# Kernel optimization log

Hardware: AMD Instinct MI355X
Metric: run time of the kernel (lower is better)

The kernel has to match this reference:

```python
import jax, jax.numpy as jnp
import numpy as np

D_STATE = 8
DT_RANK = 8  # ceil(128/16)


def _grouped_1x1(x, w):
    # x: (B,H,W,Cin), w: (g, Cout//g, Cin//g)
    B, H, W, _ = x.shape
    g, o, i = w.shape
    xg = x.reshape(B, H, W, g, i)
    return jnp.einsum('bhwgi,goi->bhwgo', xg, w).reshape(B, H, W, g * o)


def setup_inputs() -> dict:
    key = jax.random.key(0)
    ks = jax.random.split(key, 16)
    B, H, W, C = 8, 64, 64, 128
    g = 4
    D = 128  # expand_dim = d_inner
    N = D_STATE
    R = DT_RANK
    inp = {}
    inp['x'] = jax.random.normal(ks[0], (B, H, W, C), dtype=jnp.float32)
    inp['w1'] = jax.random.normal(ks[1], (g, D // g, C // g), dtype=jnp.float32) * 0.1
    inp['dw'] = jax.random.normal(ks[2], (3, 3, 1, D), dtype=jnp.float32) * 0.1  # HWIO depthwise
    inp['in_proj_w'] = jax.random.normal(ks[3], (2 * D, D), dtype=jnp.float32) * 0.05
    inp['conv1d_w'] = jax.random.normal(ks[4], (D, 3), dtype=jnp.float32) * 0.1
    inp['conv1d_b'] = jax.random.normal(ks[5], (D,), dtype=jnp.float32) * 0.05
    inp['x_proj_w'] = jax.random.normal(ks[6], (R + 2 * N, D), dtype=jnp.float32) * 0.05
    inp['dt_proj_w'] = jax.random.normal(ks[7], (D, R), dtype=jnp.float32) * 0.05
    inp['dt_proj_b'] = jax.random.normal(ks[8], (D,), dtype=jnp.float32) * 0.05
    inp['A_log'] = jnp.log(jnp.tile(jnp.arange(1, N + 1, dtype=jnp.float32)[None, :], (D, 1)))
    inp['D_param'] = jnp.ones((D,), dtype=jnp.float32)
    inp['out_proj_w'] = jax.random.normal(ks[9], (D, D), dtype=jnp.float32) * 0.05
    inp['gamma'] = jnp.ones((D,), dtype=jnp.float32)
    inp['beta'] = jnp.zeros((D,), dtype=jnp.float32)
    inp['w2'] = jax.random.normal(ks[10], (g, D // g, C // g), dtype=jnp.float32) * 0.1
    inp['wout'] = jax.random.normal(ks[11], (g, C // g, D // g), dtype=jnp.float32) * 0.1
    return inp


def _mamba(x_seq, in_proj_w, conv1d_w, conv1d_b, x_proj_w, dt_proj_w, dt_proj_b, A_log, D_param, out_proj_w):
    # x_seq: (B, L, D)
    B, L, D = x_seq.shape
    N, R = D_STATE, DT_RANK
    xz = jnp.einsum('bld,ed->ble', x_seq, in_proj_w)  # (B,L,2D)
    u, z = xz[..., :D], xz[..., D:]
    # causal depthwise conv1d, kernel=3, left pad 2 (torch: padding=2, slice [:L])
    up = jnp.pad(u, ((0, 0), (2, 0), (0, 0)))
    u = (up[:, 0:L] * conv1d_w[:, 0] + up[:, 1:L + 1] * conv1d_w[:, 1]
         + up[:, 2:L + 2] * conv1d_w[:, 2] + conv1d_b)
    u = jax.nn.silu(u)
    x_dbl = jnp.einsum('bld,ed->ble', u, x_proj_w)  # (B,L,R+2N)
    dt = x_dbl[..., :R]
    Bm = x_dbl[..., R:R + N]
    Cm = x_dbl[..., R + N:]
    delta = jax.nn.softplus(jnp.einsum('blr,dr->bld', dt, dt_proj_w) + dt_proj_b)  # (B,L,D)
    A = -jnp.exp(A_log)  # (D,N)

    def step(h, inp):
        d_t, u_t, b_t, c_t = inp  # (B,D),(B,D),(B,N),(B,N)
        dA = jnp.exp(d_t[..., None] * A)            # (B,D,N)
        h = dA * h + (d_t * u_t)[..., None] * b_t[:, None, :]
        y_t = jnp.einsum('bdn,bn->bd', h, c_t)
        return h, y_t

    h0 = jnp.zeros((B, D, N), dtype=x_seq.dtype)
    xs = (jnp.swapaxes(delta, 0, 1), jnp.swapaxes(u, 0, 1),
          jnp.swapaxes(Bm, 0, 1), jnp.swapaxes(Cm, 0, 1))
    _, ys = jax.lax.scan(step, h0, xs)              # ys: (L,B,D)
    y = jnp.swapaxes(ys, 0, 1) + u * D_param
    y = y * jax.nn.silu(z)
    return jnp.einsum('bld,ed->ble', y, out_proj_w)


def reference(x, w1, dw, in_proj_w, conv1d_w, conv1d_b, x_proj_w, dt_proj_w, dt_proj_b,
              A_log, D_param, out_proj_w, gamma, beta, w2, wout):
    B, H, W, C = x.shape
    D = dw.shape[-1]
    x1 = _grouped_1x1(x, w1)  # (B,H,W,D)
    x1 = jax.lax.conv_general_dilated(
        x1, dw, window_strides=(1, 1), padding='SAME',
        feature_group_count=D, dimension_numbers=('NHWC', 'HWIO', 'NHWC'))
    x1 = jax.nn.silu(x1)
    x1_seq = x1.reshape(B, H * W, D)
    x1_seq = _mamba(x1_seq, in_proj_w, conv1d_w, conv1d_b, x_proj_w,
                    dt_proj_w, dt_proj_b, A_log, D_param, out_proj_w)
    x1 = x1_seq.reshape(B, H, W, D)
    mu = jnp.mean(x1, axis=-1, keepdims=True)
    var = jnp.mean(jnp.square(x1 - mu), axis=-1, keepdims=True)
    x1 = (x1 - mu) * jax.lax.rsqrt(var + 1e-5) * gamma + beta
    x2 = jax.nn.silu(_grouped_1x1(x, w2))
    x_fuse = x1 * x2
    return _grouped_1x1(x_fuse, wout)  # (B,H,W,C)
```

## Files before the change

### kernel.cpp

```cpp
#include <hip/hip_runtime.h>
#include <math.h>

#define B_    8
#define C_    128
#define D_    128
#define L_    4096
#define NPOS_ 32768
#define NC_   256
#define S_    16
#define MFL_  1048576

typedef __attribute__((ext_vector_type(8))) short short8;
typedef __attribute__((ext_vector_type(4))) float f32x4;

__device__ __forceinline__ float siluf(float x) { return x / (1.f + __expf(-x)); }
__device__ __forceinline__ float softplusf(float x) {
    if (x > 20.f) return x;
    return __logf(1.f + __expf(x));
}
__device__ __forceinline__ unsigned short f2bf(float f) {
    unsigned int u = __float_as_uint(f);
    u = (u + 0x7FFFu + ((u >> 16) & 1u)) >> 16;
    return (unsigned short)u;
}
__device__ __forceinline__ float bf2f(unsigned short h) {
    return __uint_as_float(((unsigned int)h) << 16);
}
__device__ __forceinline__ void scan_as(float dl, const float* Ar, bool fast, float* a) {
    if (fast) {
        float e1 = __expf(-dl);
        a[0] = e1;
        a[1] = e1 * e1;
        a[2] = a[1] * e1;
        a[3] = a[1] * a[1];
        a[4] = a[3] * e1;
        a[5] = a[3] * a[1];
        a[6] = a[5] * e1;
        a[7] = a[3] * a[3];
    } else {
        #pragma unroll
        for (int n = 0; n < 8; ++n) a[n] = __expf(dl * Ar[n]);
    }
}

__global__ __launch_bounds__(256) void k0_cvt(const float* __restrict__ inW,
                                              const float* __restrict__ OW,
                                              const float* __restrict__ xpw,
                                              unsigned short* __restrict__ inWb,
                                              unsigned short* __restrict__ OWb,
                                              unsigned short* __restrict__ xpwb) {
    for (int i = blockIdx.x * 256 + threadIdx.x; i < 52224; i += gridDim.x * 256) {
        if (i < 32768)      inWb[i] = f2bf(inW[i]);
        else if (i < 49152) OWb[i - 32768] = f2bf(OW[i - 32768]);
        else                xpwb[i - 49152] = f2bf(xpw[i - 49152]);
    }
}

__global__ __launch_bounds__(256) void k1_g1x1(const float* __restrict__ x,
                                               const float* __restrict__ w1,
                                               const float* __restrict__ w2,
                                               unsigned short* __restrict__ t1b,
                                               unsigned short* __restrict__ x2sb) {
    __shared__ float xs[16 * 128];
    int t = threadIdx.x;
    int d = t & 127, ph = t >> 7;
    int g = d >> 5, o = d & 31;
    float w1r[32], w2r[32];
    #pragma unroll
    for (int i = 0; i < 32; ++i) {
        w1r[i] = w1[g * 1024 + o * 32 + i];
        w2r[i] = w2[g * 1024 + o * 32 + i];
    }
    int pos0 = blockIdx.x * 32;
    for (int it = 0; it < 2; ++it) {
        int p0 = pos0 + it * 16;
        #pragma unroll
        for (int q = 0; q < 2; ++q) {
            int fi = t * 2 + q;
            *(float4*)&xs[fi * 4] = *(const float4*)&x[p0 * 128 + fi * 4];
        }
        __syncthreads();
        #pragma unroll
        for (int q = 0; q < 8; ++q) {
            int pl = ph * 8 + q;
            float a1 = 0.f, a2 = 0.f;
            const float* xr = &xs[pl * 128 + g * 32];
            #pragma unroll
            for (int i4 = 0; i4 < 8; ++i4) {
                float4 xv = *(const float4*)&xr[i4 * 4];
                a1 += xv.x * w1r[i4*4] + xv.y * w1r[i4*4+1] + xv.z * w1r[i4*4+2] + xv.w * w1r[i4*4+3];
                a2 += xv.x * w2r[i4*4] + xv.y * w2r[i4*4+1] + xv.z * w2r[i4*4+2] + xv.w * w2r[i4*4+3];
            }
            int pos = p0 + pl;
            t1b[pos * 128 + d]  = f2bf(a1);
            x2sb[pos * 128 + d] = f2bf(siluf(a2));
        }
        __syncthreads();
    }
}

__global__ __launch_bounds__(128) void k2_dwconv(const unsigned short* __restrict__ t1b,
                                                 const float* __restrict__ dw,
                                                 unsigned short* __restrict__ x1cb) {
    int d = threadIdx.x;
    float dwr[9];
    #pragma unroll
    for (int k = 0; k < 9; ++k) dwr[k] = dw[k * 128 + d];
    int bid = blockIdx.x;
    int wt = bid & 15, ht = (bid >> 4) & 7, b = bid >> 7;
    int h0 = ht * 8, w0 = wt * 4;
    float rows[10][6];
    #pragma unroll
    for (int r = 0; r < 10; ++r) {
        int hh = h0 - 1 + r;
        bool hv = (hh >= 0) && (hh < 64);
        #pragma unroll
        for (int c = 0; c < 6; ++c) {
            int w = w0 - 1 + c;
            bool wvv = (w >= 0) && (w < 64);
            rows[r][c] = (hv && wvv) ? bf2f(t1b[((b * 64 + hh) * 64 + w) * 128 + d]) : 0.f;
        }
    }
    #pragma unroll
    for (int hi = 0; hi < 8; ++hi) {
        #pragma unroll
        for (int wi = 0; wi < 4; ++wi) {
            float acc = rows[hi][wi]     * dwr[0] + rows[hi][wi+1]   * dwr[1] + rows[hi][wi+2]   * dwr[2]
                      + rows[hi+1][wi]   * dwr[3] + rows[hi+1][wi+1] * dwr[4] + rows[hi+1][wi+2] * dwr[5]
                      + rows[hi+2][wi]   * dwr[6] + rows[hi+2][wi+1] * dwr[7] + rows[hi+2][wi+2] * dwr[8];
            x1cb[((b * 64 + h0 + hi) * 64 + w0 + wi) * 128 + d] = f2bf(siluf(acc));
        }
    }
}

__global__ __launch_bounds__(256) void k3_mfma(const unsigned short* __restrict__ Abf,
                                               const unsigned short* __restrict__ Bbf,
                                               unsigned short* __restrict__ urawb,
                                               unsigned short* __restrict__ zb) {
    __shared__ unsigned short Al[64 * 72];
    __shared__ unsigned short Bl[128 * 72];
    int t = threadIdx.x;
    int pos0 = (blockIdx.x >> 1) * 64;
    int half = blockIdx.x & 1;
    const unsigned short* Bh = Bbf + (size_t)half * 128 * 128;
    unsigned short* dst = half ? zb : urawb;
    int lane = t & 63, wv = t >> 6;
    int lanem = lane & 15, laneq = lane >> 4;
    f32x4 acc[8];
    #pragma unroll
    for (int i = 0; i < 8; ++i) acc[i] = (f32x4){0.f, 0.f, 0.f, 0.f};
    for (int kc = 0; kc < 2; ++kc) {
        #pragma unroll
        for (int q = 0; q < 2; ++q) {
            int c = t + q * 256;
            int row = c >> 3, col = c & 7;
            *(int4*)&Al[row * 72 + col * 8] = *(const int4*)&Abf[(pos0 + row) * 128 + kc * 64 + col * 8];
        }
        #pragma unroll
        for (int q = 0; q < 4; ++q) {
            int c = t + q * 256;
            int row = c >> 3, col = c & 7;
            *(int4*)&Bl[row * 72 + col * 8] = *(const int4*)&Bh[row * 128 + kc * 64 + col * 8];
        }
        __syncthreads();
        #pragma unroll
        for (int ks = 0; ks < 2; ++ks) {
            short8 af = *(const short8*)&Al[(wv * 16 + lanem) * 72 + ks * 32 + laneq * 8];
            #pragma unroll
            for (int ni = 0; ni < 8; ++ni) {
                short8 bfr = *(const short8*)&Bl[(ni * 16 + lanem) * 72 + ks * 32 + laneq * 8];
                acc[ni] = __builtin_amdgcn_mfma_f32_16x16x32_bf16(af, bfr, acc[ni], 0, 0, 0);
            }
        }
        __syncthreads();
    }
    #pragma unroll
    for (int ni = 0; ni < 8; ++ni)
        #pragma unroll
        for (int r = 0; r < 4; ++r) {
            int m = pos0 + wv * 16 + laneq * 4 + r;
            int n = ni * 16 + lanem;
            dst[m * 128 + n] = f2bf(acc[ni][r]);
        }
}

__global__ __launch_bounds__(256) void k4_convproj(const unsigned short* __restrict__ urawb,
                                                   const float* __restrict__ cw,
                                                   const float* __restrict__ cb,
                                                   const unsigned short* __restrict__ xpwb,
                                                   const float* __restrict__ dtw,
                                                   const float* __restrict__ dtb,
                                                   unsigned short* __restrict__ usb,
                                                   float* __restrict__ delta,
                                                   float* __restrict__ Bm,
                                                   float* __restrict__ Cm) {
    __shared__ unsigned short uA[32 * 136];
    __shared__ unsigned short xB[32 * 136];
    __shared__ float xdb[32 * 36];
    int t = threadIdx.x;
    int d = t & 127, ph = t >> 7;
    for (int i = t; i < 32 * 128; i += 256) {
        int n = i >> 7, k = i & 127;
        xB[n * 136 + k] = (n < 24) ? xpwb[n * 128 + k] : (unsigned short)0;
    }
    float cw0 = cw[d * 3 + 0], cw1 = cw[d * 3 + 1], cw2 = cw[d * 3 + 2], cbr = cb[d];
    float dtwr[8];
    #pragma unroll
    for (int r = 0; r < 8; ++r) dtwr[r] = dtw[d * 8 + r];
    float dtbr = dtb[d];

    int gpos0 = blockIdx.x * 32;
    int ll0 = (gpos0 & 4095) + ph * 16;
    int base = (gpos0 + ph * 16) * 128 + d;
    float ur0 = (ll0 >= 2) ? bf2f(urawb[base - 256]) : 0.f;
    float ur1 = (ll0 >= 1) ? bf2f(urawb[base - 128]) : 0.f;
    #pragma unroll
    for (int q = 0; q < 16; ++q) {
        float urq = bf2f(urawb[base + q * 128]);
        float v = siluf(ur0 * cw0 + ur1 * cw1 + urq * cw2 + cbr);
        unsigned short vb = f2bf(v);
        usb[base + q * 128] = vb;
        uA[(ph * 16 + q) * 136 + d] = vb;
        ur0 = ur1; ur1 = urq;
    }
    __syncthreads();
    int lane = t & 63, wv = t >> 6;
    int lanem = lane & 15, laneq = lane >> 4;
    int m0 = (wv & 1) * 16, n0 = (wv >> 1) * 16;
    f32x4 accx = (f32x4){0.f, 0.f, 0.f, 0.f};
    #pragma unroll
    for (int ks = 0; ks < 4; ++ks) {
        short8 af  = *(const short8*)&uA[(m0 + lanem) * 136 + ks * 32 + laneq * 8];
        short8 bfr = *(const short8*)&xB[(n0 + lanem) * 136 + ks * 32 + laneq * 8];
        accx = __builtin_amdgcn_mfma_f32_16x16x32_bf16(af, bfr, accx, 0, 0, 0);
    }
    #pragma unroll
    for (int r = 0; r < 4; ++r)
        xdb[(m0 + laneq * 4 + r) * 36 + n0 + lanem] = accx[r];
    __syncthreads();
    #pragma unroll
    for (int q = 0; q < 16; ++q) {
        int pl = ph * 16 + q;
        float dt = dtbr;
        #pragma unroll
        for (int r = 0; r < 8; ++r) dt += xdb[pl * 36 + r] * dtwr[r];
        delta[base + q * 128] = softplusf(dt);
    }
    for (int i = t; i < 512; i += 256) {
        int p = i >> 4, j = i & 15;
        float v = xdb[p * 36 + 8 + j];
        int gp = gpos0 + p;
        if (j < 8) Bm[gp * 8 + j] = v;
        else       Cm[gp * 8 + (j - 8)] = v;
    }
}

__global__ __launch_bounds__(128) void k5_scan1(const float* __restrict__ delta,
                                                const unsigned short* __restrict__ usb,
                                                const float* __restrict__ Bm,
                                                const float* __restrict__ A_log,
                                                float* __restrict__ cA,
                                                float* __restrict__ cB) {
    int d = threadIdx.x;
    int bc = blockIdx.x;
    int b = bc >> 8, c = bc & 255;
    float Ar[8]; bool fast = true;
    #pragma unroll
    for (int n = 0; n < 8; ++n) {
        Ar[n] = -__expf(A_log[d * 8 + n]);
        fast = fast && (fabsf(Ar[n] + (float)(n + 1)) < 2e-3f);
    }
    float h[8], ap[8];
    #pragma unroll
    for (int n = 0; n < 8; ++n) { h[n] = 0.f; ap[n] = 1.f; }
    int base  = (b * L_ + c * S_) * 128 + d;
    int bbase = (b * L_ + c * S_) * 8;
    #pragma unroll
    for (int s = 0; s < S_; ++s) {
        float dl = delta[base + s * 128];
        float uv = bf2f(usb[base + s * 128]);
        float du = dl * uv;
        float4 bm0 = *(const float4*)&Bm[bbase + s * 8];
        float4 bm1 = *(const float4*)&Bm[bbase + s * 8 + 4];
        float a[8];
        scan_as(dl, Ar, fast, a);
        ap[0] *= a[0]; h[0] = a[0] * h[0] + du * bm0.x;
        ap[1] *= a[1]; h[1] = a[1] * h[1] + du * bm0.y;
        ap[2] *= a[2]; h[2] = a[2] * h[2] + du * bm0.z;
        ap[3] *= a[3]; h[3] = a[3] * h[3] + du * bm0.w;
        ap[4] *= a[4]; h[4] = a[4] * h[4] + du * bm1.x;
        ap[5] *= a[5]; h[5] = a[5] * h[5] + du * bm1.y;
        ap[6] *= a[6]; h[6] = a[6] * h[6] + du * bm1.z;
        ap[7] *= a[7]; h[7] = a[7] * h[7] + du * bm1.w;
    }
    int obase = ((b * NC_ + c) * 128 + d) * 8;
    *(float4*)&cA[obase]     = make_float4(ap[0], ap[1], ap[2], ap[3]);
    *(float4*)&cA[obase + 4] = make_float4(ap[4], ap[5], ap[6], ap[7]);
    *(float4*)&cB[obase]     = make_float4(h[0], h[1], h[2], h[3]);
    *(float4*)&cB[obase + 4] = make_float4(h[4], h[5], h[6], h[7]);
}

__global__ __launch_bounds__(128) void k6_scan2(const float* __restrict__ cA,
                                                const float* __restrict__ cB,
                                                float* __restrict__ carry) {
    int b = blockIdx.x >> 3;
    int slice = blockIdx.x & 7;
    int dn = slice * 128 + threadIdx.x;
    float h = 0.f;
    #pragma unroll 4
    for (int c = 0; c < NC_; ++c) {
        int idx = (b * NC_ + c) * 1024 + dn;
        float a  = cA[idx];
        float bv = cB[idx];
        carry[idx] = h;
        h = a * h + bv;
    }
}

__global__ __launch_bounds__(128) void k7_scan3(const float* __restrict__ delta,
                                                const unsigned short* __restrict__ usb,
                                                const float* __restrict__ Bm,
                                                const float* __restrict__ Cm,
                                                const unsigned short* __restrict__ zb,
                                                const float* __restrict__ A_log,
                                                const float* __restrict__ Dp,
                                                const float* __restrict__ carry,
                                                unsigned short* __restrict__ ybf) {
    int d = threadIdx.x;
    int bc = blockIdx.x;
    int b = bc >> 8, c = bc & 255;
    float Ar[8]; bool fast = true;
    #pragma unroll
    for (int n = 0; n < 8; ++n) {
        Ar[n] = -__expf(A_log[d * 8 + n]);
        fast = fast && (fabsf(Ar[n] + (float)(n + 1)) < 2e-3f);
    }
    float Dpr = Dp[d];
    int cbase = ((b * NC_ + c) * 128 + d) * 8;
    float4 h0 = *(const float4*)&carry[cbase];
    float4 h1 = *(const float4*)&carry[cbase + 4];
    float h[8] = {h0.x, h0.y, h0.z, h0.w, h1.x, h1.y, h1.z, h1.w};
    int base  = (b * L_ + c * S_) * 128 + d;
    int bbase = (b * L_ + c * S_) * 8;
    #pragma unroll
    for (int s = 0; s < S_; ++s) {
        float dl = delta[base + s * 128];
        float uv = bf2f(usb[base + s * 128]);
        float zv = bf2f(zb[base + s * 128]);
        float du = dl * uv;
        float4 bm0 = *(const float4*)&Bm[bbase + s * 8];
        float4 bm1 = *(const float4*)&Bm[bbase + s * 8 + 4];
        float4 cm0 = *(const float4*)&Cm[bbase + s * 8];
        float4 cm1 = *(const float4*)&Cm[bbase + s * 8 + 4];
        float a[8];
        scan_as(dl, Ar, fast, a);
        h[0] = a[0] * h[0] + du * bm0.x;
        h[1] = a[1] * h[1] + du * bm0.y;
        h[2] = a[2] * h[2] + du * bm0.z;
        h[3] = a[3] * h[3] + du * bm0.w;
        h[4] = a[4] * h[4] + du * bm1.x;
        h[5] = a[5] * h[5] + du * bm1.y;
        h[6] = a[6] * h[6] + du * bm1.z;
        h[7] = a[7] * h[7] + du * bm1.w;
        float yv = h[0] * cm0.x + h[1] * cm0.y + h[2] * cm0.z + h[3] * cm0.w
                 + h[4] * cm1.x + h[5] * cm1.y + h[6] * cm1.z + h[7] * cm1.w;
        yv = (yv + uv * Dpr) * siluf(zv);
        ybf[base + s * 128] = f2bf(yv);
    }
}

__global__ __launch_bounds__(256) void k8a_mfma(const unsigned short* __restrict__ Abf,
                                                const unsigned short* __restrict__ Bbf,
                                                unsigned short* __restrict__ xzb) {
    __shared__ unsigned short Al[64 * 72];
    __shared__ unsigned short Bl[128 * 72];
    int t = threadIdx.x;
    int pos0 = blockIdx.x * 64;
    int lane = t & 63, wv = t >> 6;
    int lanem = lane & 15, laneq = lane >> 4;
    f32x4 acc[8];
    #pragma unroll
    for (int i = 0; i < 8; ++i) acc[i] = (f32x4){0.f, 0.f, 0.f, 0.f};
    for (int kc = 0; kc < 2; ++kc) {
        #pragma unroll
        for (int q = 0; q < 2; ++q) {
            int c = t + q * 256;
            int row = c >> 3, col = c & 7;
            *(int4*)&Al[row * 72 + col * 8] = *(const int4*)&Abf[(pos0 + row) * 128 + kc * 64 + col * 8];
        }
        #pragma unroll
        for (int q = 0; q < 4; ++q) {
            int c = t + q * 256;
            int row = c >> 3, col = c & 7;
            *(int4*)&Bl[row * 72 + col * 8] = *(const int4*)&Bbf[row * 128 + kc * 64 + col * 8];
        }
        __syncthreads();
        #pragma unroll
        for (int ks = 0; ks < 2; ++ks) {
            short8 af = *(const short8*)&Al[(wv * 16 + lanem) * 72 + ks * 32 + laneq * 8];
            #pragma unroll
            for (int ni = 0; ni < 8; ++ni) {
                short8 bfr = *(const short8*)&Bl[(ni * 16 + lanem) * 72 + ks * 32 + laneq * 8];
                acc[ni] = __builtin_amdgcn_mfma_f32_16x16x32_bf16(af, bfr, acc[ni], 0, 0, 0);
            }
        }
        __syncthreads();
    }
    #pragma unroll
    for (int ni = 0; ni < 8; ++ni)
        #pragma unroll
        for (int r = 0; r < 4; ++r) {
            int m = pos0 + wv * 16 + laneq * 4 + r;
            int n = ni * 16 + lanem;
            xzb[m * 128 + n] = f2bf(acc[ni][r]);
        }
}

__global__ __launch_bounds__(256) void k8b_epi(const unsigned short* __restrict__ xzb,
                                               const float* __restrict__ gamma,
                                               const float* __restrict__ beta,
                                               const unsigned short* __restrict__ x2sb,
                                               const float* __restrict__ wout,
                                               float* __restrict__ out) {
    __shared__ float woutL[4 * 1160];
    __shared__ float gbL[256];
    int t = threadIdx.x;
    int pos0 = blockIdx.x * 64;
    for (int idx = t; idx < 4096; idx += 256) {
        int g = idx >> 10, r = idx & 1023, o = r >> 5, i = r & 31;
        woutL[g * 1160 + o * 36 + i] = wout[idx];
    }
    if (t < 128) gbL[t] = gamma[t];
    else         gbL[t] = beta[t - 128];
    __syncthreads();

    int g = t & 3, pos = t >> 2;
    int gpos = pos0 + pos;
    float v[32];
    #pragma unroll
    for (int i4 = 0; i4 < 8; ++i4) {
        ushort4 xv = *(const ushort4*)&xzb[gpos * 128 + g * 32 + i4 * 4];
        v[i4*4+0] = bf2f(xv.x); v[i4*4+1] = bf2f(xv.y);
        v[i4*4+2] = bf2f(xv.z); v[i4*4+3] = bf2f(xv.w);
    }
    float s = 0.f, s2 = 0.f;
    #pragma unroll
    for (int i = 0; i < 32; ++i) { s += v[i]; s2 += v[i] * v[i]; }
    s  += __shfl_xor(s, 1, 64);  s  += __shfl_xor(s, 2, 64);
    s2 += __shfl_xor(s2, 1, 64); s2 += __shfl_xor(s2, 2, 64);
    float m = s * (1.f / 128.f);
    float var = s2 * (1.f / 128.f) - m * m;
    float rstd = rsqrtf(var + 1e-5f);
    #pragma unroll
    for (int i4 = 0; i4 < 8; ++i4) {
        ushort4 xv = *(const ushort4*)&x2sb[gpos * 128 + g * 32 + i4 * 4];
        unsigned short xa[4] = {xv.x, xv.y, xv.z, xv.w};
        #pragma unroll
        for (int k = 0; k < 4; ++k) {
            int e = g * 32 + i4 * 4 + k;
            float vv = (v[i4 * 4 + k] - m) * rstd * gbL[e] + gbL[128 + e];
            v[i4 * 4 + k] = vv * bf2f(xa[k]);
        }
    }
    const float* wg = &woutL[g * 1160];
    int obase = gpos * 128 + g * 32;
    #pragma unroll
    for (int ob = 0; ob < 8; ++ob) {
        float o4[4];
        #pragma unroll
        for (int oo = 0; oo < 4; ++oo) {
            int o = ob * 4 + oo;
            float acc = 0.f;
            #pragma unroll
            for (int i4 = 0; i4 < 8; ++i4) {
                float4 wv4 = *(const float4*)&wg[o * 36 + i4 * 4];
                acc += v[i4*4] * wv4.x + v[i4*4+1] * wv4.y
                     + v[i4*4+2] * wv4.z + v[i4*4+3] * wv4.w;
            }
            o4[oo] = acc;
        }
        *(float4*)&out[obase + ob * 4] = make_float4(o4[0], o4[1], o4[2], o4[3]);
    }
}

extern "C" void kernel_launch(void* const* d_in, const int* in_sizes, int n_in,
                              void* d_out, int out_size, void* d_ws, size_t ws_size,
                              hipStream_t stream) {
    (void)in_sizes; (void)n_in; (void)out_size; (void)ws_size;
    const float* x         = (const float*)d_in[0];
    const float* w1        = (const float*)d_in[1];
    const float* dw        = (const float*)d_in[2];
    const float* in_proj_w = (const float*)d_in[3];
    const float* conv1d_w  = (const float*)d_in[4];
    const float* conv1d_b  = (const float*)d_in[5];
    const float* x_proj_w  = (const float*)d_in[6];
    const float* dt_proj_w = (const float*)d_in[7];
    const float* dt_proj_b = (const float*)d_in[8];
    const float* A_log     = (const float*)d_in[9];
    const float* D_param   = (const float*)d_in[10];
    const float* out_proj_w= (const float*)d_in[11];
    const float* gamma     = (const float*)d_in[12];
    const float* beta      = (const float*)d_in[13];
    const float* w2        = (const float*)d_in[14];
    const float* wout      = (const float*)d_in[15];
    float* out = (float*)d_out;

    float* ws = (float*)d_ws;
    unsigned short* x2sb  = (unsigned short*)(ws);
    unsigned short* t1b   = (unsigned short*)(ws + 2  * (size_t)MFL_);
    unsigned short* x1cb  = (unsigned short*)(ws + 4  * (size_t)MFL_);
    unsigned short* urawb = (unsigned short*)(ws + 6  * (size_t)MFL_);
    unsigned short* zb    = (unsigned short*)(ws + 8  * (size_t)MFL_);
    unsigned short* ybf   = (unsigned short*)(ws + 10 * (size_t)MFL_);
    unsigned short* xzb   = (unsigned short*)(ws + 12 * (size_t)MFL_);
    unsigned short* usb   = (unsigned short*)(ws + 14 * (size_t)MFL_);
    float* delta = ws + 16 * (size_t)MFL_;
    float* Bm    = ws + 20 * (size_t)MFL_;
    float* Cm    = Bm + (size_t)NPOS_ * 8;
    float* cA    = Cm + (size_t)NPOS_ * 8;
    float* cB    = cA + 2 * (size_t)MFL_;
    float* carry = cB + 2 * (size_t)MFL_;
    unsigned short* inWb = (unsigned short*)(carry + 2 * (size_t)MFL_);
    unsigned short* OWb  = inWb + 32768;
    unsigned short* xpwb = OWb + 16384;

    k0_cvt<<<64, 256, 0, stream>>>(in_proj_w, out_proj_w, x_proj_w, inWb, OWb, xpwb);
    k1_g1x1<<<1024, 256, 0, stream>>>(x, w1, w2, t1b, x2sb);
    k2_dwconv<<<1024, 128, 0, stream>>>(t1b, dw, x1cb);
    k3_mfma<<<1024, 256, 0, stream>>>(x1cb, inWb, urawb, zb);
    k4_convproj<<<1024, 256, 0, stream>>>(urawb, conv1d_w, conv1d_b, xpwb,
                                          dt_proj_w, dt_proj_b, usb, delta, Bm, Cm);
    k5_scan1<<<2048, 128, 0, stream>>>(delta, usb, Bm, A_log, cA, cB);
    k6_scan2<<<64, 128, 0, stream>>>(cA, cB, carry);
    k7_scan3<<<2048, 128, 0, stream>>>(delta, usb, Bm, Cm, zb, A_log, D_param, carry, ybf);
    k8a_mfma<<<512, 256, 0, stream>>>(ybf, OWb, xzb);
    k8b_epi<<<512, 256, 0, stream>>>(xzb, gamma, beta, x2sb, wout, out);
}
```

Measured before the change: 239.6 us.

## Fuse chunk scan pass into conv/projection kernel and fold weight conversion into k1

The first-pass chunk scan (per-chunk decay products and partial states) now runs inside the conv/x_proj kernel. It reuses delta, u and B values already held in registers and shared memory instead of re-reading them from global memory in a separate kernel. The bf16 weight conversion kernel is also folded into the first grouped 1x1 kernel, with a few threads per block doing the conversion. Together these remove two kernel launches and a round of global memory traffic. The costs are more register pressure in the fused kernel and some per-block imbalance in k1.

```diff
diff --git a/kernel.cpp b/kernel.cpp
--- a/kernel.cpp
+++ b/kernel.cpp
@@ -43,26 +43,27 @@
     }
 }
 
-__global__ __launch_bounds__(256) void k0_cvt(const float* __restrict__ inW,
-                                              const float* __restrict__ OW,
-                                              const float* __restrict__ xpw,
-                                              unsigned short* __restrict__ inWb,
-                                              unsigned short* __restrict__ OWb,
-                                              unsigned short* __restrict__ xpwb) {
-    for (int i = blockIdx.x * 256 + threadIdx.x; i < 52224; i += gridDim.x * 256) {
-        if (i < 32768)      inWb[i] = f2bf(inW[i]);
-        else if (i < 49152) OWb[i - 32768] = f2bf(OW[i - 32768]);
-        else                xpwb[i - 49152] = f2bf(xpw[i - 49152]);
-    }
-}
-
 __global__ __launch_bounds__(256) void k1_g1x1(const float* __restrict__ x,
                                                const float* __restrict__ w1,
                                                const float* __restrict__ w2,
+                                               const float* __restrict__ inW,
+                                               const float* __restrict__ OW,
+                                               const float* __restrict__ xpw,
+                                               unsigned short* __restrict__ inWb,
+                                               unsigned short* __restrict__ OWb,
+                                               unsigned short* __restrict__ xpwb,
                                                unsigned short* __restrict__ t1b,
                                                unsigned short* __restrict__ x2sb) {
     __shared__ float xs[16 * 128];
     int t = threadIdx.x;
+    {
+        int i = blockIdx.x * 51 + t;
+        if (t < 51 && i < 52224) {
+            if (i < 32768)      inWb[i] = f2bf(inW[i]);
+            else if (i < 49152) OWb[i - 32768] = f2bf(OW[i - 32768]);
+            else                xpwb[i - 49152] = f2bf(xpw[i - 49152]);
+        }
+    }
     int d = t & 127, ph = t >> 7;
     int g = d >> 5, o = d & 31;
     float w1r[32], w2r[32];
@@ -184,16 +185,19 @@
         }
 }
 
-__global__ __launch_bounds__(256) void k4_convproj(const unsigned short* __restrict__ urawb,
-                                                   const float* __restrict__ cw,
-                                                   const float* __restrict__ cb,
-                                                   const unsigned short* __restrict__ xpwb,
-                                                   const float* __restrict__ dtw,
-                                                   const float* __restrict__ dtb,
-                                                   unsigned short* __restrict__ usb,
-                                                   float* __restrict__ delta,
-                                                   float* __restrict__ Bm,
-                                                   float* __restrict__ Cm) {
+__global__ __launch_bounds__(256) void k45_convproj(const unsigned short* __restrict__ urawb,
+                                                    const float* __restrict__ cw,
+                                                    const float* __restrict__ cb,
+                                                    const unsigned short* __restrict__ xpwb,
+                                                    const float* __restrict__ dtw,
+                                                    const float* __restrict__ dtb,
+                                                    const float* __restrict__ A_log,
+                                                    unsigned short* __restrict__ usb,
+                                                    float* __restrict__ delta,
+                                                    float* __restrict__ Bm,
+                                                    float* __restrict__ Cm,
+                                                    float* __restrict__ cA,
+                                                    float* __restrict__ cB) {
     __shared__ unsigned short uA[32 * 136];
     __shared__ unsigned short xB[32 * 136];
     __shared__ float xdb[32 * 36];
@@ -208,6 +212,12 @@
     #pragma unroll
     for (int r = 0; r < 8; ++r) dtwr[r] = dtw[d * 8 + r];
     float dtbr = dtb[d];
+    float Ar[8]; bool fast = true;
+    #pragma unroll
+    for (int n = 0; n < 8; ++n) {
+        Ar[n] = -__expf(A_log[d * 8 + n]);
+        fast = fast && (fabsf(Ar[n] + (float)(n + 1)) < 2e-3f);
+    }
 
     int gpos0 = blockIdx.x * 32;
     int ll0 = (gpos0 & 4095) + ph * 16;
@@ -238,14 +248,33 @@
     for (int r = 0; r < 4; ++r)
         xdb[(m0 + laneq * 4 + r) * 36 + n0 + lanem] = accx[r];
     __syncthreads();
+    float h[8], ap[8];
+    #pragma unroll
+    for (int n = 0; n < 8; ++n) { h[n] = 0.f; ap[n] = 1.f; }
     #pragma unroll
     for (int q = 0; q < 16; ++q) {
         int pl = ph * 16 + q;
         float dt = dtbr;
         #pragma unroll
         for (int r = 0; r < 8; ++r) dt += xdb[pl * 36 + r] * dtwr[r];
-        delta[base + q * 128] = softplusf(dt);
-    }
+        float dl = softplusf(dt);
+        delta[base + q * 128] = dl;
+        float du = dl * bf2f(uA[pl * 136 + d]);
+        float a[8];
+        scan_as(dl, Ar, fast, a);
+        #pragma unroll
+        for (int n = 0; n < 8; ++n) {
+            ap[n] *= a[n];
+            h[n] = a[n] * h[n] + du * xdb[pl * 36 + 8 + n];
+        }
+    }
+    int bH = gpos0 >> 12;
+    int c  = ((gpos0 & 4095) >> 4) + ph;
+    int obase = ((bH * NC_ + c) * 128 + d) * 8;
+    *(float4*)&cA[obase]     = make_float4(ap[0], ap[1], ap[2], ap[3]);
+    *(float4*)&cA[obase + 4] = make_float4(ap[4], ap[5], ap[6], ap[7]);
+    *(float4*)&cB[obase]     = make_float4(h[0], h[1], h[2], h[3]);
+    *(float4*)&cB[obase + 4] = make_float4(h[4], h[5], h[6], h[7]);
     for (int i = t; i < 512; i += 256) {
         int p = i >> 4, j = i & 15;
         float v = xdb[p * 36 + 8 + j];
@@ -253,51 +282,6 @@
         if (j < 8) Bm[gp * 8 + j] = v;
         else       Cm[gp * 8 + (j - 8)] = v;
     }
-}
-
-__global__ __launch_bounds__(128) void k5_scan1(const float* __restrict__ delta,
-                                                const unsigned short* __restrict__ usb,
-                                                const float* __restrict__ Bm,
-                                                const float* __restrict__ A_log,
-                                                float* __restrict__ cA,
-                                                float* __restrict__ cB) {
-    int d = threadIdx.x;
-    int bc = blockIdx.x;
-    int b = bc >> 8, c = bc & 255;
-    float Ar[8]; bool fast = true;
-    #pragma unroll
-    for (int n = 0; n < 8; ++n) {
-        Ar[n] = -__expf(A_log[d * 8 + n]);
-        fast = fast && (fabsf(Ar[n] + (float)(n + 1)) < 2e-3f);
-    }
-    float h[8], ap[8];
-    #pragma unroll
-    for (int n = 0; n < 8; ++n) { h[n] = 0.f; ap[n] = 1.f; }
-    int base  = (b * L_ + c * S_) * 128 + d;
-    int bbase = (b * L_ + c * S_) * 8;
-    #pragma unroll
-    for (int s = 0; s < S_; ++s) {
-        float dl = delta[base + s * 128];
-        float uv = bf2f(usb[base + s * 128]);
-        float du = dl * uv;
-        float4 bm0 = *(const float4*)&Bm[bbase + s * 8];
-        float4 bm1 = *(const float4*)&Bm[bbase + s * 8 + 4];
-        float a[8];
-        scan_as(dl, Ar, fast, a);
-        ap[0] *= a[0]; h[0] = a[0] * h[0] + du * bm0.x;
-        ap[1] *= a[1]; h[1] = a[1] * h[1] + du * bm0.y;
-        ap[2] *= a[2]; h[2] = a[2] * h[2] + du * bm0.z;
-        ap[3] *= a[3]; h[3] = a[3] * h[3] + du * bm0.w;
-        ap[4] *= a[4]; h[4] = a[4] * h[4] + du * bm1.x;
-        ap[5] *= a[5]; h[5] = a[5] * h[5] + du * bm1.y;
-        ap[6] *= a[6]; h[6] = a[6] * h[6] + du * bm1.z;
-        ap[7] *= a[7]; h[7] = a[7] * h[7] + du * bm1.w;
-    }
-    int obase = ((b * NC_ + c) * 128 + d) * 8;
-    *(float4*)&cA[obase]     = make_float4(ap[0], ap[1], ap[2], ap[3]);
-    *(float4*)&cA[obase + 4] = make_float4(ap[4], ap[5], ap[6], ap[7]);
-    *(float4*)&cB[obase]     = make_float4(h[0], h[1], h[2], h[3]);
-    *(float4*)&cB[obase + 4] = make_float4(h[4], h[5], h[6], h[7]);
 }
 
 __global__ __launch_bounds__(128) void k6_scan2(const float* __restrict__ cA,
@@ -524,13 +508,13 @@
     unsigned short* OWb  = inWb + 32768;
     unsigned short* xpwb = OWb + 16384;
 
-    k0_cvt<<<64, 256, 0, stream>>>(in_proj_w, out_proj_w, x_proj_w, inWb, OWb, xpwb);
-    k1_g1x1<<<1024, 256, 0, stream>>>(x, w1, w2, t1b, x2sb);
+    k1_g1x1<<<1024, 256, 0, stream>>>(x, w1, w2, in_proj_w, out_proj_w, x_proj_w,
+                                      inWb, OWb, xpwb, t1b, x2sb);
     k2_dwconv<<<1024, 128, 0, stream>>>(t1b, dw, x1cb);
     k3_mfma<<<1024, 256, 0, stream>>>(x1cb, inWb, urawb, zb);
-    k4_convproj<<<1024, 256, 0, stream>>>(urawb, conv1d_w, conv1d_b, xpwb,
-                                          dt_proj_w, dt_proj_b, usb, delta, Bm, Cm);
-    k5_scan1<<<2048, 128, 0, stream>>>(delta, usb, Bm, A_log, cA, cB);
+    k45_convproj<<<1024, 256, 0, stream>>>(urawb, conv1d_w, conv1d_b, xpwb,
+                                           dt_proj_w, dt_proj_b, A_log,
+                                           usb, delta, Bm, Cm, cA, cB);
     k6_scan2<<<64, 128, 0, stream>>>(cA, cB, carry);
     k7_scan3<<<2048, 128, 0, stream>>>(delta, usb, Bm, Cm, zb, A_log, D_param, carry, ybf);
     k8a_mfma<<<512, 256, 0, stream>>>(ybf, OWb, xzb);
```

New measurement: 237.5 us. Within noise of the previous version (-0.9%).
